# Optimization experiments

Hardware: AMD Instinct MI355X
Metric: run time of the kernel (lower is better)

Reference implementation:

```python
import jax, jax.numpy as jnp
import numpy as np

D_MODEL = 1024
D_PROJ = D_MODEL // 4


def setup_inputs() -> dict:
    key = jax.random.key(0)
    k1, k2, k3 = jax.random.split(key, 3)
    hidden_states = jax.random.normal(k1, (4, 2048, D_MODEL), dtype=jnp.float32)
    proj_w = jax.random.normal(k2, (D_PROJ, D_MODEL), dtype=jnp.float32) * 0.02
    proj_b = jnp.zeros((D_PROJ,), dtype=jnp.float32)
    clf_w = jax.random.normal(k3, (1, 1), dtype=jnp.float32) * 0.02
    clf_b = jnp.zeros((1,), dtype=jnp.float32)
    return {"hidden_states": hidden_states, "proj_w": proj_w, "proj_b": proj_b,
            "clf_w": clf_w, "clf_b": clf_b}


def reference(hidden_states, proj_w, proj_b, clf_w, clf_b):
    # h: [B, S, D/4]
    h = jax.nn.relu(jnp.einsum('bsd,pd->bsp', hidden_states, proj_w) + proj_b)
    # pairwise dot products == batched h @ h^T: [B, S, S]
    scores = jnp.einsum('bip,bjp->bij', h, h)
    # scalar affine classifier (Linear(1,1)) folded in
    return scores * clf_w[0, 0] + clf_b[0]
```

## Files before the change

kernel.cpp:

```cpp
#include <hip/hip_runtime.h>
#include <hip/hip_bf16.h>

typedef __bf16 bf16_t;
typedef __attribute__((ext_vector_type(8))) __bf16 bf16x8;
typedef __attribute__((ext_vector_type(4))) float f32x4;

#define SEQ    2048
#define DMODEL 1024
#define DPROJ  256
#define NBATCH 4

__device__ __forceinline__ bf16x8 cvt8(const float4& lo, const float4& hi) {
    bf16x8 v;
    v[0] = (bf16_t)lo.x; v[1] = (bf16_t)lo.y; v[2] = (bf16_t)lo.z; v[3] = (bf16_t)lo.w;
    v[4] = (bf16_t)hi.x; v[5] = (bf16_t)hi.y; v[6] = (bf16_t)hi.z; v[7] = (bf16_t)hi.w;
    return v;
}

__global__ __launch_bounds__(256) void proj_kernel(
    const float* __restrict__ X, const float* __restrict__ W,
    const float* __restrict__ bias, bf16_t* __restrict__ H)
{
    __shared__ __align__(16) bf16_t As[64][40];
    __shared__ __align__(16) bf16_t Bs[64][40];

    const int m0 = blockIdx.x * 64;
    const int n0 = blockIdx.y * 64;
    const int tid  = threadIdx.x;
    const int lane = tid & 63;
    const int wave = tid >> 6;
    const int quad = lane >> 4;
    const int l16  = lane & 15;
    const int wm = (wave & 1) * 32;
    const int wn = (wave >> 1) * 32;

    const int srow = tid >> 2;
    const int scol = (tid & 3) * 8;

    f32x4 acc[2][2] = {};

    for (int k0 = 0; k0 < DMODEL; k0 += 32) {
        const float* ga = X + (size_t)(m0 + srow) * DMODEL + k0 + scol;
        float4 alo = *(const float4*)ga;
        float4 ahi = *(const float4*)(ga + 4);
        const float* gw = W + (size_t)(n0 + srow) * DMODEL + k0 + scol;
        float4 wlo = *(const float4*)gw;
        float4 whi = *(const float4*)(gw + 4);
        __syncthreads();
        *(bf16x8*)&As[srow][scol] = cvt8(alo, ahi);
        *(bf16x8*)&Bs[srow][scol] = cvt8(wlo, whi);
        __syncthreads();
        bf16x8 af[2], bf[2];
        #pragma unroll
        for (int i = 0; i < 2; ++i) {
            af[i] = *(const bf16x8*)&As[wm + i * 16 + l16][quad * 8];
            bf[i] = *(const bf16x8*)&Bs[wn + i * 16 + l16][quad * 8];
        }
        #pragma unroll
        for (int i = 0; i < 2; ++i)
            #pragma unroll
            for (int j = 0; j < 2; ++j)
                acc[i][j] = __builtin_amdgcn_mfma_f32_16x16x32_bf16(
                    af[i], bf[j], acc[i][j], 0, 0, 0);
    }

    #pragma unroll
    for (int i = 0; i < 2; ++i) {
        #pragma unroll
        for (int j = 0; j < 2; ++j) {
            const int gn = n0 + wn + j * 16 + l16;
            const float bv = bias[gn];
            #pragma unroll
            for (int r = 0; r < 4; ++r) {
                const int gm = m0 + wm + i * 16 + quad * 4 + r;
                float v = acc[i][j][r] + bv;
                v = v > 0.f ? v : 0.f;
                H[(size_t)gm * DPROJ + gn] = (bf16_t)v;
            }
        }
    }
}

__global__ __launch_bounds__(256) void score_kernel(
    const bf16_t* __restrict__ H, const float* __restrict__ clf_w,
    const float* __restrict__ clf_b, float* __restrict__ Out)
{
    __shared__ __align__(16) bf16_t As[64][40];
    __shared__ __align__(16) bf16_t Bs[64][40];

    const int b  = blockIdx.z;
    const int m0 = blockIdx.x * 64;
    const int n0 = blockIdx.y * 64;
    const bf16_t* Hb = H + (size_t)b * SEQ * DPROJ;
    float* Ob = Out + (size_t)b * SEQ * SEQ;

    const int tid  = threadIdx.x;
    const int lane = tid & 63;
    const int wave = tid >> 6;
    const int quad = lane >> 4;
    const int l16  = lane & 15;
    const int wm = (wave & 1) * 32;
    const int wn = (wave >> 1) * 32;
    const int srow = tid >> 2;
    const int scol = (tid & 3) * 8;

    f32x4 acc[2][2] = {};

    for (int k0 = 0; k0 < DPROJ; k0 += 32) {
        uint4 av = *(const uint4*)(Hb + (size_t)(m0 + srow) * DPROJ + k0 + scol);
        uint4 bv = *(const uint4*)(Hb + (size_t)(n0 + srow) * DPROJ + k0 + scol);
        __syncthreads();
        *(uint4*)&As[srow][scol] = av;
        *(uint4*)&Bs[srow][scol] = bv;
        __syncthreads();
        bf16x8 af[2], bf[2];
        #pragma unroll
        for (int i = 0; i < 2; ++i) {
            af[i] = *(const bf16x8*)&As[wm + i * 16 + l16][quad * 8];
            bf[i] = *(const bf16x8*)&Bs[wn + i * 16 + l16][quad * 8];
        }
        #pragma unroll
        for (int i = 0; i < 2; ++i)
            #pragma unroll
            for (int j = 0; j < 2; ++j)
                acc[i][j] = __builtin_amdgcn_mfma_f32_16x16x32_bf16(
                    af[i], bf[j], acc[i][j], 0, 0, 0);
    }

    const float scale = clf_w[0];
    const float off   = clf_b[0];
    #pragma unroll
    for (int i = 0; i < 2; ++i)
        #pragma unroll
        for (int j = 0; j < 2; ++j)
            #pragma unroll
            for (int r = 0; r < 4; ++r) {
                const int gm = m0 + wm + i * 16 + quad * 4 + r;
                const int gn = n0 + wn + j * 16 + l16;
                Ob[(size_t)gm * SEQ + gn] = acc[i][j][r] * scale + off;
            }
}

extern "C" void kernel_launch(void* const* d_in, const int* in_sizes, int n_in,
                              void* d_out, int out_size, void* d_ws, size_t ws_size,
                              hipStream_t stream) {
    const float* X    = (const float*)d_in[0];
    const float* W    = (const float*)d_in[1];
    const float* bias = (const float*)d_in[2];
    const float* clfw = (const float*)d_in[3];
    const float* clfb = (const float*)d_in[4];
    float* Out = (float*)d_out;
    bf16_t* H  = (bf16_t*)d_ws;

    dim3 g1(NBATCH * SEQ / 64, DPROJ / 64, 1);
    proj_kernel<<<g1, 256, 0, stream>>>(X, W, bias, H);

    dim3 g2(SEQ / 64, SEQ / 64, NBATCH);
    score_kernel<<<g2, 256, 0, stream>>>(H, clfw, clfb, Out);
}
```

Measured before the change: 138.3 us.

## Enlarge GEMM tiles and use direct global-to-LDS loads with swizzle

The projection kernel widens its N tile to 128 so each X tile is converted and reused across twice as many output columns. The score kernel moves to 128x128 tiles with a 64-wide K step, loading H straight into LDS through global_load_lds with an XOR swizzle that avoids bank conflicts. This cuts redundant global reads of H and X and removes register staging for the score GEMM. In exchange it raises per-thread accumulator registers and halves the number of blocks, which can lower occupancy.

```diff
diff --git a/kernel.cpp b/kernel.cpp
--- a/kernel.cpp
+++ b/kernel.cpp
@@ -17,57 +17,70 @@
     return v;
 }
 
+__device__ __forceinline__ void gl_lds16(const void* g, void* l) {
+    __builtin_amdgcn_global_load_lds(
+        (const __attribute__((address_space(1))) unsigned int*)g,
+        (__attribute__((address_space(3))) unsigned int*)l, 16, 0, 0);
+}
+
 __global__ __launch_bounds__(256) void proj_kernel(
     const float* __restrict__ X, const float* __restrict__ W,
     const float* __restrict__ bias, bf16_t* __restrict__ H)
 {
-    __shared__ __align__(16) bf16_t As[64][40];
-    __shared__ __align__(16) bf16_t Bs[64][40];
+    __shared__ __align__(16) bf16_t Xs[64][40];
+    __shared__ __align__(16) bf16_t Ws[128][40];
 
     const int m0 = blockIdx.x * 64;
-    const int n0 = blockIdx.y * 64;
+    const int n0 = blockIdx.y * 128;
     const int tid  = threadIdx.x;
     const int lane = tid & 63;
     const int wave = tid >> 6;
     const int quad = lane >> 4;
     const int l16  = lane & 15;
     const int wm = (wave & 1) * 32;
-    const int wn = (wave >> 1) * 32;
+    const int wn = (wave >> 1) * 64;
 
-    const int srow = tid >> 2;
-    const int scol = (tid & 3) * 8;
+    const int xrow = tid >> 2;
+    const int xcol = (tid & 3) * 8;
+    const int wrow = tid >> 1;
+    const int wcol = (tid & 1) * 16;
 
-    f32x4 acc[2][2] = {};
+    f32x4 acc[2][4] = {};
 
     for (int k0 = 0; k0 < DMODEL; k0 += 32) {
-        const float* ga = X + (size_t)(m0 + srow) * DMODEL + k0 + scol;
-        float4 alo = *(const float4*)ga;
-        float4 ahi = *(const float4*)(ga + 4);
-        const float* gw = W + (size_t)(n0 + srow) * DMODEL + k0 + scol;
-        float4 wlo = *(const float4*)gw;
-        float4 whi = *(const float4*)(gw + 4);
+        const float* gx = X + (size_t)(m0 + xrow) * DMODEL + k0 + xcol;
+        float4 x0 = *(const float4*)gx;
+        float4 x1 = *(const float4*)(gx + 4);
+        const float* gw = W + (size_t)(n0 + wrow) * DMODEL + k0 + wcol;
+        float4 w0 = *(const float4*)gw;
+        float4 w1 = *(const float4*)(gw + 4);
+        float4 w2 = *(const float4*)(gw + 8);
+        float4 w3 = *(const float4*)(gw + 12);
         __syncthreads();
-        *(bf16x8*)&As[srow][scol] = cvt8(alo, ahi);
-        *(bf16x8*)&Bs[srow][scol] = cvt8(wlo, whi);
+        *(bf16x8*)&Xs[xrow][xcol]     = cvt8(x0, x1);
+        *(bf16x8*)&Ws[wrow][wcol]     = cvt8(w0, w1);
+        *(bf16x8*)&Ws[wrow][wcol + 8] = cvt8(w2, w3);
         __syncthreads();
-        bf16x8 af[2], bf[2];
+
+        bf16x8 af[2], bfr[4];
         #pragma unroll
-        for (int i = 0; i < 2; ++i) {
-            af[i] = *(const bf16x8*)&As[wm + i * 16 + l16][quad * 8];
-            bf[i] = *(const bf16x8*)&Bs[wn + i * 16 + l16][quad * 8];
-        }
+        for (int i = 0; i < 2; ++i)
+            af[i] = *(const bf16x8*)&Xs[wm + i * 16 + l16][quad * 8];
+        #pragma unroll
+        for (int j = 0; j < 4; ++j)
+            bfr[j] = *(const bf16x8*)&Ws[wn + j * 16 + l16][quad * 8];
         #pragma unroll
         for (int i = 0; i < 2; ++i)
             #pragma unroll
-            for (int j = 0; j < 2; ++j)
+            for (int j = 0; j < 4; ++j)
                 acc[i][j] = __builtin_amdgcn_mfma_f32_16x16x32_bf16(
-                    af[i], bf[j], acc[i][j], 0, 0, 0);
+                    af[i], bfr[j], acc[i][j], 0, 0, 0);
     }
 
     #pragma unroll
     for (int i = 0; i < 2; ++i) {
         #pragma unroll
-        for (int j = 0; j < 2; ++j) {
+        for (int j = 0; j < 4; ++j) {
             const int gn = n0 + wn + j * 16 + l16;
             const float bv = bias[gn];
             #pragma unroll
@@ -85,12 +98,12 @@
     const bf16_t* __restrict__ H, const float* __restrict__ clf_w,
     const float* __restrict__ clf_b, float* __restrict__ Out)
 {
-    __shared__ __align__(16) bf16_t As[64][40];
-    __shared__ __align__(16) bf16_t Bs[64][40];
+    __shared__ __align__(16) bf16_t As[128 * 64];
+    __shared__ __align__(16) bf16_t Bs[128 * 64];
 
     const int b  = blockIdx.z;
-    const int m0 = blockIdx.x * 64;
-    const int n0 = blockIdx.y * 64;
+    const int m0 = blockIdx.x * 128;
+    const int n0 = blockIdx.y * 128;
     const bf16_t* Hb = H + (size_t)b * SEQ * DPROJ;
     float* Ob = Out + (size_t)b * SEQ * SEQ;
 
@@ -99,40 +112,63 @@
     const int wave = tid >> 6;
     const int quad = lane >> 4;
     const int l16  = lane & 15;
-    const int wm = (wave & 1) * 32;
-    const int wn = (wave >> 1) * 32;
-    const int srow = tid >> 2;
-    const int scol = (tid & 3) * 8;
+    const int wm = (wave & 1) * 64;
+    const int wn = (wave >> 1) * 64;
+    const int swz = l16 & 7;
 
-    f32x4 acc[2][2] = {};
+    const bf16_t* gA[4];
+    const bf16_t* gB[4];
+    bf16_t* lA[4];
+    bf16_t* lB[4];
+    #pragma unroll
+    for (int t = 0; t < 4; ++t) {
+        const int g   = (wave * 4 + t) * 64 + lane;
+        const int row = g >> 3;
+        const int gc  = (g & 7) ^ (row & 7);
+        gA[t] = Hb + (size_t)(m0 + row) * DPROJ + gc * 8;
+        gB[t] = Hb + (size_t)(n0 + row) * DPROJ + gc * 8;
+        lA[t] = As + (wave * 4 + t) * 512;
+        lB[t] = Bs + (wave * 4 + t) * 512;
+    }
 
-    for (int k0 = 0; k0 < DPROJ; k0 += 32) {
-        uint4 av = *(const uint4*)(Hb + (size_t)(m0 + srow) * DPROJ + k0 + scol);
-        uint4 bv = *(const uint4*)(Hb + (size_t)(n0 + srow) * DPROJ + k0 + scol);
+    f32x4 acc[4][4] = {};
+
+    for (int kt = 0; kt < 4; ++kt) {
         __syncthreads();
-        *(uint4*)&As[srow][scol] = av;
-        *(uint4*)&Bs[srow][scol] = bv;
+        #pragma unroll
+        for (int t = 0; t < 4; ++t) {
+            gl_lds16(gA[t], lA[t]);
+            gl_lds16(gB[t], lB[t]);
+        }
         __syncthreads();
-        bf16x8 af[2], bf[2];
         #pragma unroll
-        for (int i = 0; i < 2; ++i) {
-            af[i] = *(const bf16x8*)&As[wm + i * 16 + l16][quad * 8];
-            bf[i] = *(const bf16x8*)&Bs[wn + i * 16 + l16][quad * 8];
+        for (int t = 0; t < 4; ++t) { gA[t] += 64; gB[t] += 64; }
+
+        #pragma unroll
+        for (int s = 0; s < 2; ++s) {
+            const int ch = ((s * 4 + quad) ^ swz) * 8;
+            bf16x8 af[4], bfr[4];
+            #pragma unroll
+            for (int i = 0; i < 4; ++i)
+                af[i] = *(const bf16x8*)&As[(wm + i * 16 + l16) * 64 + ch];
+            #pragma unroll
+            for (int j = 0; j < 4; ++j)
+                bfr[j] = *(const bf16x8*)&Bs[(wn + j * 16 + l16) * 64 + ch];
+            #pragma unroll
+            for (int i = 0; i < 4; ++i)
+                #pragma unroll
+                for (int j = 0; j < 4; ++j)
+                    acc[i][j] = __builtin_amdgcn_mfma_f32_16x16x32_bf16(
+                        af[i], bfr[j], acc[i][j], 0, 0, 0);
         }
-        #pragma unroll
-        for (int i = 0; i < 2; ++i)
-            #pragma unroll
-            for (int j = 0; j < 2; ++j)
-                acc[i][j] = __builtin_amdgcn_mfma_f32_16x16x32_bf16(
-                    af[i], bf[j], acc[i][j], 0, 0, 0);
     }
 
     const float scale = clf_w[0];
     const float off   = clf_b[0];
     #pragma unroll
-    for (int i = 0; i < 2; ++i)
+    for (int i = 0; i < 4; ++i)
         #pragma unroll
-        for (int j = 0; j < 2; ++j)
+        for (int j = 0; j < 4; ++j)
             #pragma unroll
             for (int r = 0; r < 4; ++r) {
                 const int gm = m0 + wm + i * 16 + quad * 4 + r;
@@ -152,9 +188,9 @@
     float* Out = (float*)d_out;
     bf16_t* H  = (bf16_t*)d_ws;
 
-    dim3 g1(NBATCH * SEQ / 64, DPROJ / 64, 1);
+    dim3 g1(NBATCH * SEQ / 64, DPROJ / 128, 1);
     proj_kernel<<<g1, 256, 0, stream>>>(X, W, bias, H);
 
-    dim3 g2(SEQ / 64, SEQ / 64, NBATCH);
+    dim3 g2(SEQ / 128, SEQ / 128, NBATCH);
     score_kernel<<<g2, 256, 0, stream>>>(H, clfw, clfb, Out);
 }
```

New measurement: 137.6 us. Within noise of the previous version (-0.5%).
